# Kernel optimization log

Measured on AMD Instinct MI355X. Metric: run time of the kernel, lower is better.

## Reference

```python
import jax, jax.numpy as jnp
import numpy as np

NS, NV = 16, 4          # scalar / vector multiplicities (model defaults)
N_NODES, N_EDGES = 50000, 400000
WEIGHT_NUMEL = NS * NS + NS * NV  # 320: paths 0e*0e->0e and 0e*1o->1o


def sph_harm_l012(vec):
    """Real spherical harmonics l=0,1,2 with e3nn 'component' normalization,
    evaluated on the normalized edge vectors. Output [E, 9]."""
    eps = 1e-8
    r = vec / (jnp.linalg.norm(vec, axis=-1, keepdims=True) + eps)
    x, y, z = r[:, 0], r[:, 1], r[:, 2]
    sh0 = jnp.ones_like(x)[:, None]
    c1 = np.float32(np.sqrt(3.0))
    sh1 = c1 * jnp.stack([x, y, z], -1)
    c2 = np.float32(np.sqrt(15.0))
    c2b = np.float32(np.sqrt(5.0) / 2.0)
    sh2 = jnp.stack([c2 * x * y, c2 * y * z, c2b * (3 * z * z - 1.0),
                     c2 * z * x, 0.5 * c2 * (x * x - y * y)], -1)
    return jnp.concatenate([sh0, sh1, sh2], -1)


def setup_inputs() -> dict:
    key = jax.random.key(0)
    ks = jax.random.split(key, 8)
    h = 3 * NS  # n_edge_features = hidden_features = 48
    node_attr = jax.random.normal(ks[0], (N_NODES, NS), jnp.float32)
    edge_attr = jax.random.normal(ks[1], (N_EDGES, h), jnp.float32)
    edge_vec = jax.random.normal(ks[2], (N_EDGES, 3), jnp.float32)
    edge_index = jax.random.randint(ks[3], (2, N_EDGES), 0, N_NODES)
    fc1_w = jax.random.normal(ks[4], (h, h), jnp.float32) / np.sqrt(h)
    fc1_b = jnp.zeros((h,), jnp.float32)
    fc2_w = jax.random.normal(ks[5], (h, WEIGHT_NUMEL), jnp.float32) / np.sqrt(h)
    fc2_b = jnp.zeros((WEIGHT_NUMEL,), jnp.float32)
    return {"node_attr": node_attr, "edge_attr": edge_attr, "edge_vec": edge_vec,
            "fc1_w": fc1_w, "fc1_b": fc1_b, "fc2_w": fc2_w, "fc2_b": fc2_b,
            "edge_index": edge_index}


def reference(node_attr, edge_attr, edge_vec, fc1_w, fc1_b, fc2_w, fc2_b, edge_index):
    N = node_attr.shape[0]
    E = edge_attr.shape[0]
    edge_src, edge_dst = edge_index[0], edge_index[1]

    # spherical harmonics of edge directions (build_*_conv_graph)
    edge_sh = sph_harm_l012(edge_vec)                 # [E, 9]

    # per-edge TP weights: fc = Linear -> ReLU -> Linear (dropout=0)
    w = jax.nn.relu(edge_attr @ fc1_w + fc1_b) @ fc2_w + fc2_b  # [E, 320]
    w0 = w[:, :NS * NS].reshape(E, NS, NS)            # path 0e x 0e -> 0e
    w1 = w[:, NS * NS:].reshape(E, NS, NV)            # path 0e x 1o -> 1o

    # gather destination-node features
    x = node_attr[edge_dst]                           # [E, NS]

    # FullyConnectedTensorProduct('16x0e', sh, '16x0e + 4x1o'):
    # fan-in per output = NS (mul_u * mul_v summed over paths) -> 1/sqrt(NS)
    inv = np.float32(1.0 / np.sqrt(NS))
    out0 = jnp.einsum('euw,eu->ew', w0, x) * edge_sh[:, :1] * inv       # [E, NS]
    out1 = jnp.einsum('euw,eu,em->ewm', w1, x, edge_sh[:, 1:4]) * inv   # [E, NV, 3]
    msg = jnp.concatenate([out0, out1.reshape(E, NV * 3)], -1)          # [E, NS+3*NV]

    # scatter-mean over edge_src (reduce='mean', dim_size=N)
    summed = jax.ops.segment_sum(msg, edge_src, num_segments=N)
    cnt = jax.ops.segment_sum(jnp.ones((E,), msg.dtype), edge_src, num_segments=N)
    return summed / jnp.maximum(cnt, 1.0)[:, None]
```

## Files before the change

### kernel.cpp

```cpp
#include <hip/hip_runtime.h>
#include <hip/hip_bf16.h>
#include <math.h>

#define NS 16
#define H  48
#define TB 256
#define THREADS 512

typedef __attribute__((ext_vector_type(8))) short bf16x8;
typedef __attribute__((ext_vector_type(4))) float f32x4;

#define W2O   2304
#define B1H   20224
#define ZO    20272
#define ATO   20280
#define XO_   36664
#define SMEM_HW 40760
#define MSGF  10140
#define WCPY  2535

__device__ __forceinline__ short f2bf(float f) {
    unsigned b = __float_as_uint(f);
    unsigned r = (b + 0x7FFFu + ((b >> 16) & 1u)) >> 16;
    return (short)r;
}
__device__ __forceinline__ float bf2f(short s) {
    return __uint_as_float(((unsigned)(unsigned short)s) << 16);
}
__device__ __forceinline__ unsigned cvtpk(float lo, float hi) {
    unsigned r;
    asm("v_cvt_pk_bf16_f32 %0, %1, %2" : "=v"(r) : "v"(lo), "v"(hi));
    return r;
}
__device__ __forceinline__ uint4 pk8(float4 a, float4 b) {
    uint4 q;
    q.x = cvtpk(a.x, a.y); q.y = cvtpk(a.z, a.w);
    q.z = cvtpk(b.x, b.y); q.w = cvtpk(b.z, b.w);
    return q;
}

__global__ __launch_bounds__(256) void prep_hist_kernel(
    const float* __restrict__ fc1_w, const float* __restrict__ fc2_w,
    const float* __restrict__ fc1_b, const float* __restrict__ fc2_b,
    short* __restrict__ wpack,
    const int* __restrict__ edge_index, int* __restrict__ deg, int E)
{
    if (blockIdx.x < 6) {
        int t = blockIdx.x * 256 + threadIdx.x;
        if (t < 1472) {
            int f = t >> 6, l = t & 63;
            bool isW1 = (f < 3);
            int u = isW1 ? f : (f - 3);
            int n = u * 16 + (l & 15);
            const float* W = isW1 ? fc1_w : fc2_w;
            int ldw = isW1 ? 48 : 320;
            int base = isW1 ? (f * 768) : (W2O + u * 896);
            short* d0 = wpack + base + l * 8;
            #pragma unroll
            for (int i = 0; i < 8; ++i)
                d0[i] = f2bf(W[((l >> 4) * 8 + i) * ldw + n]);
            if (l < 32) {
                short* d1 = wpack + base + 512 + l * 8;
                #pragma unroll
                for (int i = 0; i < 8; ++i)
                    d1[i] = f2bf(W[(32 + (l >> 4) * 8 + i) * ldw + n]);
            } else if (!isW1 && l < 48) {
                short* d1 = wpack + base + 512 + l * 8;
                d1[0] = f2bf(fc2_b[n]);
                #pragma unroll
                for (int i = 1; i < 8; ++i) d1[i] = 0;
            }
        } else if (t < 1520) {
            wpack[B1H + (t - 1472)] = f2bf(fc1_b[t - 1472]);
        } else if (t < 1528) {
            wpack[ZO + (t - 1520)] = 0;
        }
    } else {
        int i = (blockIdx.x - 6) * 256 + threadIdx.x;
        if (i < E) atomicAdd(deg + edge_index[i], 1);
    }
}

__global__ __launch_bounds__(THREADS, 2) void edge_mfma_kernel(
    const float* __restrict__ node_attr,
    const float* __restrict__ edge_attr,
    const float* __restrict__ edge_vec,
    const short* __restrict__ wpack,
    const int*   __restrict__ edge_index,
    float* __restrict__ msg,
    int*   __restrict__ cursor,
    int E)
{
    __shared__ __align__(16) short smemS[SMEM_HW];
    float* smemF = (float*)smemS;
    const int tid = threadIdx.x;
    const int base = blockIdx.x * TB;
    const int l  = tid & 63;
    const int wv = tid >> 6;
    const int g  = l >> 4;
    const int c  = l & 15;
    const int rb = wv * 32;

    const int r = tid >> 1, h = tid & 1;
    const int e = base + r;
    const int ce = e < E ? e : (E - 1);
    const int sI_raw = edge_index[ce];
    const int dI = edge_index[E + ce];

    float shx_r = 0.f, shy_r = 0.f, shz_r = 0.f;
    int slot_r = 0;

    for (int idx = tid; idx < WCPY; idx += THREADS) {
        uint4 v = ((const uint4*)wpack)[idx];
        *(uint4*)&smemS[idx * 8] = v;
    }

    {
        const float* ap = edge_attr + (size_t)ce * H + h * 24;
        float4 A0 = *(const float4*)(ap + 0);
        float4 A1 = *(const float4*)(ap + 4);
        float4 A2 = *(const float4*)(ap + 8);
        float4 A3 = *(const float4*)(ap + 12);
        float4 A4 = *(const float4*)(ap + 16);
        float4 A5 = *(const float4*)(ap + 20);
        const float* xp = node_attr + (size_t)dI * NS + h * 8;
        float4 X0 = *(const float4*)(xp + 0);
        float4 X1 = *(const float4*)(xp + 4);
        if (e >= E) {
            A0 = make_float4(0,0,0,0); A1 = A0; A2 = A0; A3 = A0; A4 = A0; A5 = A0;
            X0 = A0; X1 = A0;
        }
        const int s8 = (r & 7) << 3;
        *(uint4*)&smemS[ATO + r * 64 + (((h*3 + 0) << 3) ^ s8)] = pk8(A0, A1);
        *(uint4*)&smemS[ATO + r * 64 + (((h*3 + 1) << 3) ^ s8)] = pk8(A2, A3);
        *(uint4*)&smemS[ATO + r * 64 + (((h*3 + 2) << 3) ^ s8)] = pk8(A4, A5);
        {
            int az = ATO + r * 64 + (((6 + h) << 3) ^ s8);
            uint4 zq;
            zq.x = (h == 0) ? 0x00003F80u : 0u;
            zq.y = 0u; zq.z = 0u; zq.w = 0u;
            *(uint4*)&smemS[az] = zq;
        }
        *(uint4*)&smemS[XO_ + r * 16 + h * 8] = pk8(X0, X1);
        if (h == 0) {
            int sI = (e < E) ? sI_raw : 0;
            float vx = 0.f, vy = 0.f, vz = 0.f;
            if (e < E) {
                vx = edge_vec[3 * (size_t)ce + 0];
                vy = edge_vec[3 * (size_t)ce + 1];
                vz = edge_vec[3 * (size_t)ce + 2];
            }
            float rn = 1.0f / (sqrtf(vx*vx + vy*vy + vz*vz) + 1e-8f);
            const float c1 = 1.7320508075688772f;
            shx_r = c1 * vx * rn; shy_r = c1 * vy * rn; shz_r = c1 * vz * rn;
            if (e < E) slot_r = atomicAdd(cursor + sI, 1);
        }
    }
    __syncthreads();

    bf16x8 a0[2], a1[2];
    #pragma unroll
    for (int m = 0; m < 2; ++m) {
        int row = rb + m * 16 + c, s8 = (row & 7) << 3;
        a0[m] = *(const bf16x8*)&smemS[ATO + row * 64 + ((g * 8) ^ s8)];
        a1[m] = *(const bf16x8*)&smemS[ATO + row * 64 + ((32 + g * 8) ^ s8)];
    }
    #pragma unroll
    for (int fr = 0; fr < 3; ++fr) {
        bf16x8 b0 = *(const bf16x8*)&smemS[fr * 768 + l * 8];
        bf16x8 b1 = *(const bf16x8*)&smemS[(l < 32) ? (fr * 768 + 512 + l * 8) : ZO];
        float bia = bf2f(smemS[B1H + fr * 16 + c]);
        #pragma unroll
        for (int m = 0; m < 2; ++m) {
            f32x4 acc = {0.f, 0.f, 0.f, 0.f};
            acc = __builtin_amdgcn_mfma_f32_16x16x32_bf16(a0[m], b0, acc, 0, 0, 0);
            acc = __builtin_amdgcn_mfma_f32_16x16x32_bf16(a1[m], b1, acc, 0, 0, 0);
            float t0 = fmaxf(acc[0] + bia, 0.f);
            float t1 = fmaxf(acc[1] + bia, 0.f);
            float t2 = fmaxf(acc[2] + bia, 0.f);
            float t3 = fmaxf(acc[3] + bia, 0.f);
            unsigned p01 = cvtpk(t0, t1);
            unsigned p23 = cvtpk(t2, t3);
            int row0 = rb + m * 16 + g * 4;
            int col = fr * 16 + c;
            smemS[ATO + (row0+0) * 64 + (col ^ (((row0+0) & 7) << 3))] = (short)p01;
            smemS[ATO + (row0+1) * 64 + (col ^ (((row0+1) & 7) << 3))] = (short)(p01 >> 16);
            smemS[ATO + (row0+2) * 64 + (col ^ (((row0+2) & 7) << 3))] = (short)p23;
            smemS[ATO + (row0+3) * 64 + (col ^ (((row0+3) & 7) << 3))] = (short)(p23 >> 16);
        }
    }

    bf16x8 tf0[2], tf1[2];
    #pragma unroll
    for (int m = 0; m < 2; ++m) {
        int row = rb + m * 16 + c, s8 = (row & 7) << 3;
        tf0[m] = *(const bf16x8*)&smemS[ATO + row * 64 + ((g * 8) ^ s8)];
        tf1[m] = *(const bf16x8*)&smemS[ATO + row * 64 + ((32 + g * 8) ^ s8)];
    }
    bf16x8 xr0[2][4], xr1[2][4];
    #pragma unroll
    for (int m = 0; m < 2; ++m)
        #pragma unroll
        for (int j = 0; j < 4; ++j) {
            int row = rb + m * 16 + g * 4 + j;
            xr0[m][j] = *(const bf16x8*)&smemS[XO_ + row * 16];
            xr1[m][j] = *(const bf16x8*)&smemS[XO_ + row * 16 + 8];
        }

    float o0[2][4] = {{0.f,0.f,0.f,0.f},{0.f,0.f,0.f,0.f}};
    float o1[2][4] = {{0.f,0.f,0.f,0.f},{0.f,0.f,0.f,0.f}};
    const int s2 = c >> 2;
    #pragma unroll
    for (int u = 0; u < 20; ++u) {
        const int wb = W2O + u * 896;
        bf16x8 b0 = *(const bf16x8*)&smemS[wb + l * 8];
        bf16x8 b1 = *(const bf16x8*)&smemS[(l < 48) ? (wb + 512 + l * 8) : ZO];
        #pragma unroll
        for (int m = 0; m < 2; ++m) {
            f32x4 acc = {0.f, 0.f, 0.f, 0.f};
            acc = __builtin_amdgcn_mfma_f32_16x16x32_bf16(tf0[m], b0, acc, 0, 0, 0);
            acc = __builtin_amdgcn_mfma_f32_16x16x32_bf16(tf1[m], b1, acc, 0, 0, 0);
            if (u < 16) {
                #pragma unroll
                for (int j = 0; j < 4; ++j) {
                    float xu = bf2f(u < 8 ? xr0[m][j][u] : xr1[m][j][u - 8]);
                    o0[m][j] = fmaf(xu, acc[j], o0[m][j]);
                }
            } else {
                const int f = u - 16;
                #pragma unroll
                for (int j = 0; j < 4; ++j) {
                    float e0, e1, e2, e3;
                    if (f < 2) {
                        e0 = bf2f(xr0[m][j][f*4+0]); e1 = bf2f(xr0[m][j][f*4+1]);
                        e2 = bf2f(xr0[m][j][f*4+2]); e3 = bf2f(xr0[m][j][f*4+3]);
                    } else {
                        e0 = bf2f(xr1[m][j][(f-2)*4+0]); e1 = bf2f(xr1[m][j][(f-2)*4+1]);
                        e2 = bf2f(xr1[m][j][(f-2)*4+2]); e3 = bf2f(xr1[m][j][(f-2)*4+3]);
                    }
                    float xu = e0;
                    xu = (s2 == 1) ? e1 : xu;
                    xu = (s2 == 2) ? e2 : xu;
                    xu = (s2 == 3) ? e3 : xu;
                    o1[m][j] = fmaf(xu, acc[j], o1[m][j]);
                }
            }
        }
    }
    #pragma unroll
    for (int m = 0; m < 2; ++m)
        #pragma unroll
        for (int j = 0; j < 4; ++j) {
            o1[m][j] += __shfl_xor(o1[m][j], 4);
            o1[m][j] += __shfl_xor(o1[m][j], 8);
        }

    const float inv = 0.25f;
    #pragma unroll
    for (int m = 0; m < 2; ++m)
        #pragma unroll
        for (int j = 0; j < 4; ++j) {
            const int rloc = m*16 + g*4 + j;
            const int rr = rb + rloc;
            const int srcl = rloc * 2;
            float shx = __shfl(shx_r, srcl);
            float shy = __shfl(shy_r, srcl);
            float shz = __shfl(shz_r, srcl);
            int lsrc = (g << 4) + (c < 12 ? c / 3 : 0);
            float ov = __shfl(o1[m][j], lsrc);
            int m3 = c - 3 * (c / 3);
            float shm = (m3 == 0) ? shx : ((m3 == 1) ? shy : shz);
            float v2 = (c < 12) ? ov * shm * inv : 0.f;
            smemF[MSGF + rr * 32 + c]      = o0[m][j] * inv;
            smemF[MSGF + rr * 32 + 16 + c] = v2;
        }

    #pragma unroll
    for (int it = 0; it < 4; ++it) {
        int rloc2 = it * 8 + (l >> 3);
        int r2 = rb + rloc2;
        int ch = (l & 7) * 4;
        int e2 = base + r2;
        int slot = __shfl(slot_r, rloc2 * 2);
        float4 val = *(const float4*)&smemF[MSGF + r2 * 32 + ch];
        if (e2 < E) *(float4*)(msg + (size_t)slot * 32 + ch) = val;
    }
}

__global__ __launch_bounds__(1024) void offsets_kernel(
    const int* __restrict__ deg, int* __restrict__ starts,
    int* __restrict__ cursor, int* __restrict__ gtotal, int N)
{
    __shared__ int lds[1024];
    __shared__ int base_s;
    const int t = threadIdx.x;
    const int i = blockIdx.x * 1024 + t;
    int v = (i < N) ? deg[i] : 0;
    lds[t] = v;
    __syncthreads();
    int acc = v;
    for (int off = 1; off < 1024; off <<= 1) {
        int u = (t >= off) ? lds[t - off] : 0;
        __syncthreads();
        acc += u;
        lds[t] = acc;
        __syncthreads();
    }
    if (t == 1023) base_s = atomicAdd(gtotal, acc);
    __syncthreads();
    int excl = acc - v;
    if (i < N) {
        int s = base_s + excl;
        starts[i] = s;
        cursor[i] = s;
    }
}

__global__ __launch_bounds__(256) void sum_kernel(
    const float* __restrict__ msg, const int* __restrict__ starts,
    const int* __restrict__ deg, float* __restrict__ out, int N)
{
    int n = (blockIdx.x * blockDim.x + threadIdx.x) >> 5;
    int ch = threadIdx.x & 31;
    if (n >= N) return;
    int s = starts[n], d = deg[n];
    const float* mb = msg + (size_t)s * 32 + ch;
    float a0 = 0.f, a1 = 0.f, a2 = 0.f, a3 = 0.f;
    int k = 0;
    for (; k + 4 <= d; k += 4) {
        a0 += mb[(size_t)(k + 0) * 32];
        a1 += mb[(size_t)(k + 1) * 32];
        a2 += mb[(size_t)(k + 2) * 32];
        a3 += mb[(size_t)(k + 3) * 32];
    }
    if (k + 2 <= d) {
        a0 += mb[(size_t)(k + 0) * 32];
        a1 += mb[(size_t)(k + 1) * 32];
        k += 2;
    }
    if (k < d) a2 += mb[(size_t)k * 32];
    float acc = (a0 + a1) + (a2 + a3);
    if (ch < 28) out[(size_t)n * 28 + ch] = acc / fmaxf((float)d, 1.0f);
}

__global__ __launch_bounds__(256) void finalize_kernel(
    float* __restrict__ out, const float* __restrict__ cnt, int total)
{
    int i = blockIdx.x * blockDim.x + threadIdx.x;
    if (i < total) {
        float cv = cnt[i / 28];
        out[i] = out[i] / fmaxf(cv, 1.0f);
    }
}

__global__ __launch_bounds__(256) void naive_kernel(
    const float* __restrict__ node_attr, const float* __restrict__ edge_attr,
    const float* __restrict__ edge_vec, const float* __restrict__ fc1_w,
    const float* __restrict__ fc1_b, const float* __restrict__ fc2_w,
    const float* __restrict__ fc2_b, const int* __restrict__ edge_index,
    float* __restrict__ out, float* __restrict__ cnt, int E)
{
    int e = blockIdx.x * blockDim.x + threadIdx.x;
    if (e >= E) return;
    float a[H];
    for (int i = 0; i < H; ++i) a[i] = edge_attr[(size_t)e*H + i];
    int dst = edge_index[E + e];
    float x[NS];
    for (int i = 0; i < NS; ++i) x[i] = node_attr[(size_t)dst*NS + i];
    float o0[NS] = {0}, o1v[4] = {0};
    for (int k = 0; k < H; ++k) {
        float tk = fc1_b[k];
        for (int j = 0; j < H; ++j) tk = fmaf(a[j], fc1_w[j*H + k], tk);
        tk = fmaxf(tk, 0.f);
        const float* row = fc2_w + k*320;
        for (int u = 0; u < NS; ++u) {
            float q = tk * x[u];
            for (int w = 0; w < NS; ++w) o0[w] = fmaf(q, row[u*NS+w], o0[w]);
            for (int v = 0; v < 4; ++v) o1v[v] = fmaf(q, row[256+u*4+v], o1v[v]);
        }
    }
    for (int u = 0; u < NS; ++u) {
        float xu = x[u];
        for (int w = 0; w < NS; ++w) o0[w] = fmaf(xu, fc2_b[u*NS+w], o0[w]);
        for (int v = 0; v < 4; ++v) o1v[v] = fmaf(xu, fc2_b[256+u*4+v], o1v[v]);
    }
    float vx = edge_vec[3*(size_t)e], vy = edge_vec[3*(size_t)e+1], vz = edge_vec[3*(size_t)e+2];
    float rn = 1.0f / (sqrtf(vx*vx+vy*vy+vz*vz) + 1e-8f);
    const float c1 = 1.7320508075688772f;
    float sx = c1*vx*rn, sy = c1*vy*rn, sz = c1*vz*rn;
    int src = edge_index[e];
    float* ob = out + (size_t)src * 28;
    for (int w = 0; w < NS; ++w) atomicAdd(ob + w, o0[w] * 0.25f);
    for (int v = 0; v < 4; ++v) {
        float q = o1v[v] * 0.25f;
        atomicAdd(ob + 16 + 3*v + 0, q * sx);
        atomicAdd(ob + 16 + 3*v + 1, q * sy);
        atomicAdd(ob + 16 + 3*v + 2, q * sz);
    }
    atomicAdd(cnt + src, 1.0f);
}

extern "C" void kernel_launch(void* const* d_in, const int* in_sizes, int n_in,
                              void* d_out, int out_size, void* d_ws, size_t ws_size,
                              hipStream_t stream) {
    const float* node_attr  = (const float*)d_in[0];
    const float* edge_attr  = (const float*)d_in[1];
    const float* edge_vec   = (const float*)d_in[2];
    const float* fc1_w      = (const float*)d_in[3];
    const float* fc1_b      = (const float*)d_in[4];
    const float* fc2_w      = (const float*)d_in[5];
    const float* fc2_b      = (const float*)d_in[6];
    const int*   edge_index = (const int*)d_in[7];

    int E = in_sizes[2] / 3;
    int N = in_sizes[0] / NS;
    float* out = (float*)d_out;

    size_t msg_b  = (size_t)E * 32 * sizeof(float);
    size_t ints_b = (3 * (size_t)N + 1) * sizeof(int);
    size_t wpk_b  = (size_t)WCPY * 16;
    size_t need   = msg_b + ints_b + wpk_b;

    if (ws_size >= need) {
        float* msg  = (float*)d_ws;
        int* ip     = (int*)((char*)d_ws + msg_b);
        int* deg    = ip;
        int* gtotal = ip + N;
        int* starts = ip + N + 1;
        int* cursor = ip + 2 * N + 1;
        short* wpack = (short*)((char*)d_ws + msg_b + ints_b);

        hipMemsetAsync(deg, 0, ((size_t)N + 1) * sizeof(int), stream);
        int nhist = (E + 255) / 256;
        prep_hist_kernel<<<6 + nhist, 256, 0, stream>>>(
            fc1_w, fc2_w, fc1_b, fc2_b, wpack, edge_index, deg, E);
        offsets_kernel<<<(N + 1023) / 1024, 1024, 0, stream>>>(
            deg, starts, cursor, gtotal, N);
        edge_mfma_kernel<<<(E + TB - 1) / TB, THREADS, 0, stream>>>(
            node_attr, edge_attr, edge_vec, wpack, edge_index, msg, cursor, E);
        sum_kernel<<<((size_t)N * 32 + 255) / 256, 256, 0, stream>>>(
            msg, starts, deg, out, N);
    } else {
        float* cnt = (float*)d_ws;
        hipMemsetAsync(d_out, 0, (size_t)out_size * sizeof(float), stream);
        hipMemsetAsync(d_ws, 0, (size_t)N * sizeof(float), stream);
        naive_kernel<<<(E + 255) / 256, 256, 0, stream>>>(
            node_attr, edge_attr, edge_vec, fc1_w, fc1_b, fc2_w, fc2_b,
            edge_index, out, cnt, E);
        int total = N * 28;
        finalize_kernel<<<(total + 255) / 256, 256, 0, stream>>>(out, cnt, total);
    }
}
```

Measured before the change: 104.4 us.

## Shrink edge tile to 64 edges per block with four loader threads per edge

Shrinks each block from 256 edges on 512 threads to 64 edges on 256 threads, so every wave handles one 16-row MFMA tile instead of two. Loading changes to four threads per edge: three threads fetch edge_attr slices and the fourth fetches node features, the edge vector and the zero padding. The goal is lower register and LDS use per block, which allows more resident blocks and more latency hiding on the gathers. The trade-off is that the 2535-vector packed weight table is copied into LDS by four times as many blocks, each with half the threads, and each B fragment loaded from LDS now feeds one MFMA tile instead of two.

```diff
diff --git a/kernel.cpp b/kernel.cpp
--- a/kernel.cpp
+++ b/kernel.cpp
@@ -4,8 +4,8 @@
 
 #define NS 16
 #define H  48
-#define TB 256
-#define THREADS 512
+#define TB 64
+#define THREADS 256
 
 typedef __attribute__((ext_vector_type(8))) short bf16x8;
 typedef __attribute__((ext_vector_type(4))) float f32x4;
@@ -14,8 +14,8 @@
 #define B1H   20224
 #define ZO    20272
 #define ATO   20280
-#define XO_   36664
-#define SMEM_HW 40760
+#define XO_   24376
+#define SMEM_HW 25400
 #define MSGF  10140
 #define WCPY  2535
 
@@ -99,9 +99,9 @@
     const int wv = tid >> 6;
     const int g  = l >> 4;
     const int c  = l & 15;
-    const int rb = wv * 32;
-
-    const int r = tid >> 1, h = tid & 1;
+    const int rb = wv * 16;
+
+    const int r = tid >> 2, h = tid & 3;
     const int e = base + r;
     const int ce = e < E ? e : (E - 1);
     const int sI_raw = edge_index[ce];
@@ -116,34 +116,31 @@
     }
 
     {
-        const float* ap = edge_attr + (size_t)ce * H + h * 24;
-        float4 A0 = *(const float4*)(ap + 0);
-        float4 A1 = *(const float4*)(ap + 4);
-        float4 A2 = *(const float4*)(ap + 8);
-        float4 A3 = *(const float4*)(ap + 12);
-        float4 A4 = *(const float4*)(ap + 16);
-        float4 A5 = *(const float4*)(ap + 20);
-        const float* xp = node_attr + (size_t)dI * NS + h * 8;
-        float4 X0 = *(const float4*)(xp + 0);
-        float4 X1 = *(const float4*)(xp + 4);
-        if (e >= E) {
-            A0 = make_float4(0,0,0,0); A1 = A0; A2 = A0; A3 = A0; A4 = A0; A5 = A0;
-            X0 = A0; X1 = A0;
-        }
         const int s8 = (r & 7) << 3;
-        *(uint4*)&smemS[ATO + r * 64 + (((h*3 + 0) << 3) ^ s8)] = pk8(A0, A1);
-        *(uint4*)&smemS[ATO + r * 64 + (((h*3 + 1) << 3) ^ s8)] = pk8(A2, A3);
-        *(uint4*)&smemS[ATO + r * 64 + (((h*3 + 2) << 3) ^ s8)] = pk8(A4, A5);
-        {
-            int az = ATO + r * 64 + (((6 + h) << 3) ^ s8);
-            uint4 zq;
-            zq.x = (h == 0) ? 0x00003F80u : 0u;
-            zq.y = 0u; zq.z = 0u; zq.w = 0u;
-            *(uint4*)&smemS[az] = zq;
-        }
-        *(uint4*)&smemS[XO_ + r * 16 + h * 8] = pk8(X0, X1);
-        if (h == 0) {
-            int sI = (e < E) ? sI_raw : 0;
+        if (h < 3) {
+            const float* ap = edge_attr + (size_t)ce * H + h * 16;
+            float4 A0 = *(const float4*)(ap + 0);
+            float4 A1 = *(const float4*)(ap + 4);
+            float4 A2 = *(const float4*)(ap + 8);
+            float4 A3 = *(const float4*)(ap + 12);
+            if (e >= E) {
+                A0 = make_float4(0,0,0,0); A1 = A0; A2 = A0; A3 = A0;
+            }
+            *(uint4*)&smemS[ATO + r * 64 + (((2*h + 0) << 3) ^ s8)] = pk8(A0, A1);
+            *(uint4*)&smemS[ATO + r * 64 + (((2*h + 1) << 3) ^ s8)] = pk8(A2, A3);
+        } else {
+            uint4 zq; zq.x = 0x00003F80u; zq.y = 0u; zq.z = 0u; zq.w = 0u;
+            uint4 zz; zz.x = 0u; zz.y = 0u; zz.z = 0u; zz.w = 0u;
+            *(uint4*)&smemS[ATO + r * 64 + ((6 << 3) ^ s8)] = zq;
+            *(uint4*)&smemS[ATO + r * 64 + ((7 << 3) ^ s8)] = zz;
+            const float* xp = node_attr + (size_t)dI * NS;
+            float4 X0 = *(const float4*)(xp + 0);
+            float4 X1 = *(const float4*)(xp + 4);
+            float4 X2 = *(const float4*)(xp + 8);
+            float4 X3 = *(const float4*)(xp + 12);
+            if (e >= E) { X0 = make_float4(0,0,0,0); X1 = X0; X2 = X0; X3 = X0; }
+            *(uint4*)&smemS[XO_ + r * 16 + 0] = pk8(X0, X1);
+            *(uint4*)&smemS[XO_ + r * 16 + 8] = pk8(X2, X3);
             float vx = 0.f, vy = 0.f, vz = 0.f;
             if (e < E) {
                 vx = edge_vec[3 * (size_t)ce + 0];
@@ -153,135 +150,113 @@
             float rn = 1.0f / (sqrtf(vx*vx + vy*vy + vz*vz) + 1e-8f);
             const float c1 = 1.7320508075688772f;
             shx_r = c1 * vx * rn; shy_r = c1 * vy * rn; shz_r = c1 * vz * rn;
-            if (e < E) slot_r = atomicAdd(cursor + sI, 1);
         }
+        if (h == 0 && e < E) slot_r = atomicAdd(cursor + sI_raw, 1);
     }
     __syncthreads();
 
-    bf16x8 a0[2], a1[2];
-    #pragma unroll
-    for (int m = 0; m < 2; ++m) {
-        int row = rb + m * 16 + c, s8 = (row & 7) << 3;
-        a0[m] = *(const bf16x8*)&smemS[ATO + row * 64 + ((g * 8) ^ s8)];
-        a1[m] = *(const bf16x8*)&smemS[ATO + row * 64 + ((32 + g * 8) ^ s8)];
-    }
+    const int rowA = rb + c, s8a = (rowA & 7) << 3;
+    bf16x8 a0 = *(const bf16x8*)&smemS[ATO + rowA * 64 + ((g * 8) ^ s8a)];
+    bf16x8 a1 = *(const bf16x8*)&smemS[ATO + rowA * 64 + ((32 + g * 8) ^ s8a)];
     #pragma unroll
     for (int fr = 0; fr < 3; ++fr) {
         bf16x8 b0 = *(const bf16x8*)&smemS[fr * 768 + l * 8];
         bf16x8 b1 = *(const bf16x8*)&smemS[(l < 32) ? (fr * 768 + 512 + l * 8) : ZO];
         float bia = bf2f(smemS[B1H + fr * 16 + c]);
-        #pragma unroll
-        for (int m = 0; m < 2; ++m) {
-            f32x4 acc = {0.f, 0.f, 0.f, 0.f};
-            acc = __builtin_amdgcn_mfma_f32_16x16x32_bf16(a0[m], b0, acc, 0, 0, 0);
-            acc = __builtin_amdgcn_mfma_f32_16x16x32_bf16(a1[m], b1, acc, 0, 0, 0);
-            float t0 = fmaxf(acc[0] + bia, 0.f);
-            float t1 = fmaxf(acc[1] + bia, 0.f);
-            float t2 = fmaxf(acc[2] + bia, 0.f);
-            float t3 = fmaxf(acc[3] + bia, 0.f);
-            unsigned p01 = cvtpk(t0, t1);
-            unsigned p23 = cvtpk(t2, t3);
-            int row0 = rb + m * 16 + g * 4;
-            int col = fr * 16 + c;
-            smemS[ATO + (row0+0) * 64 + (col ^ (((row0+0) & 7) << 3))] = (short)p01;
-            smemS[ATO + (row0+1) * 64 + (col ^ (((row0+1) & 7) << 3))] = (short)(p01 >> 16);
-            smemS[ATO + (row0+2) * 64 + (col ^ (((row0+2) & 7) << 3))] = (short)p23;
-            smemS[ATO + (row0+3) * 64 + (col ^ (((row0+3) & 7) << 3))] = (short)(p23 >> 16);
-        }
-    }
-
-    bf16x8 tf0[2], tf1[2];
-    #pragma unroll
-    for (int m = 0; m < 2; ++m) {
-        int row = rb + m * 16 + c, s8 = (row & 7) << 3;
-        tf0[m] = *(const bf16x8*)&smemS[ATO + row * 64 + ((g * 8) ^ s8)];
-        tf1[m] = *(const bf16x8*)&smemS[ATO + row * 64 + ((32 + g * 8) ^ s8)];
-    }
-    bf16x8 xr0[2][4], xr1[2][4];
-    #pragma unroll
-    for (int m = 0; m < 2; ++m)
-        #pragma unroll
-        for (int j = 0; j < 4; ++j) {
-            int row = rb + m * 16 + g * 4 + j;
-            xr0[m][j] = *(const bf16x8*)&smemS[XO_ + row * 16];
-            xr1[m][j] = *(const bf16x8*)&smemS[XO_ + row * 16 + 8];
-        }
-
-    float o0[2][4] = {{0.f,0.f,0.f,0.f},{0.f,0.f,0.f,0.f}};
-    float o1[2][4] = {{0.f,0.f,0.f,0.f},{0.f,0.f,0.f,0.f}};
+        f32x4 acc = {0.f, 0.f, 0.f, 0.f};
+        acc = __builtin_amdgcn_mfma_f32_16x16x32_bf16(a0, b0, acc, 0, 0, 0);
+        acc = __builtin_amdgcn_mfma_f32_16x16x32_bf16(a1, b1, acc, 0, 0, 0);
+        float t0 = fmaxf(acc[0] + bia, 0.f);
+        float t1 = fmaxf(acc[1] + bia, 0.f);
+        float t2 = fmaxf(acc[2] + bia, 0.f);
+        float t3 = fmaxf(acc[3] + bia, 0.f);
+        unsigned p01 = cvtpk(t0, t1);
+        unsigned p23 = cvtpk(t2, t3);
+        int row0 = rb + g * 4;
+        int col = fr * 16 + c;
+        smemS[ATO + (row0+0) * 64 + (col ^ (((row0+0) & 7) << 3))] = (short)p01;
+        smemS[ATO + (row0+1) * 64 + (col ^ (((row0+1) & 7) << 3))] = (short)(p01 >> 16);
+        smemS[ATO + (row0+2) * 64 + (col ^ (((row0+2) & 7) << 3))] = (short)p23;
+        smemS[ATO + (row0+3) * 64 + (col ^ (((row0+3) & 7) << 3))] = (short)(p23 >> 16);
+    }
+
+    bf16x8 tf0 = *(const bf16x8*)&smemS[ATO + rowA * 64 + ((g * 8) ^ s8a)];
+    bf16x8 tf1 = *(const bf16x8*)&smemS[ATO + rowA * 64 + ((32 + g * 8) ^ s8a)];
+    bf16x8 xr0[4], xr1[4];
+    #pragma unroll
+    for (int j = 0; j < 4; ++j) {
+        int row = rb + g * 4 + j;
+        xr0[j] = *(const bf16x8*)&smemS[XO_ + row * 16];
+        xr1[j] = *(const bf16x8*)&smemS[XO_ + row * 16 + 8];
+    }
+
+    float o0[4] = {0.f, 0.f, 0.f, 0.f};
+    float o1[4] = {0.f, 0.f, 0.f, 0.f};
     const int s2 = c >> 2;
     #pragma unroll
     for (int u = 0; u < 20; ++u) {
         const int wb = W2O + u * 896;
         bf16x8 b0 = *(const bf16x8*)&smemS[wb + l * 8];
         bf16x8 b1 = *(const bf16x8*)&smemS[(l < 48) ? (wb + 512 + l * 8) : ZO];
-        #pragma unroll
-        for (int m = 0; m < 2; ++m) {
-            f32x4 acc = {0.f, 0.f, 0.f, 0.f};
-            acc = __builtin_amdgcn_mfma_f32_16x16x32_bf16(tf0[m], b0, acc, 0, 0, 0);
-            acc = __builtin_amdgcn_mfma_f32_16x16x32_bf16(tf1[m], b1, acc, 0, 0, 0);
-            if (u < 16) {
-                #pragma unroll
-                for (int j = 0; j < 4; ++j) {
-                    float xu = bf2f(u < 8 ? xr0[m][j][u] : xr1[m][j][u - 8]);
-                    o0[m][j] = fmaf(xu, acc[j], o0[m][j]);
+        f32x4 acc = {0.f, 0.f, 0.f, 0.f};
+        acc = __builtin_amdgcn_mfma_f32_16x16x32_bf16(tf0, b0, acc, 0, 0, 0);
+        acc = __builtin_amdgcn_mfma_f32_16x16x32_bf16(tf1, b1, acc, 0, 0, 0);
+        if (u < 16) {
+            #pragma unroll
+            for (int j = 0; j < 4; ++j) {
+                float xu = bf2f(u < 8 ? xr0[j][u] : xr1[j][u - 8]);
+                o0[j] = fmaf(xu, acc[j], o0[j]);
+            }
+        } else {
+            const int f = u - 16;
+            #pragma unroll
+            for (int j = 0; j < 4; ++j) {
+                float e0, e1, e2, e3;
+                if (f < 2) {
+                    e0 = bf2f(xr0[j][f*4+0]); e1 = bf2f(xr0[j][f*4+1]);
+                    e2 = bf2f(xr0[j][f*4+2]); e3 = bf2f(xr0[j][f*4+3]);
+                } else {
+                    e0 = bf2f(xr1[j][(f-2)*4+0]); e1 = bf2f(xr1[j][(f-2)*4+1]);
+                    e2 = bf2f(xr1[j][(f-2)*4+2]); e3 = bf2f(xr1[j][(f-2)*4+3]);
                 }
-            } else {
-                const int f = u - 16;
-                #pragma unroll
-                for (int j = 0; j < 4; ++j) {
-                    float e0, e1, e2, e3;
-                    if (f < 2) {
-                        e0 = bf2f(xr0[m][j][f*4+0]); e1 = bf2f(xr0[m][j][f*4+1]);
-                        e2 = bf2f(xr0[m][j][f*4+2]); e3 = bf2f(xr0[m][j][f*4+3]);
-                    } else {
-                        e0 = bf2f(xr1[m][j][(f-2)*4+0]); e1 = bf2f(xr1[m][j][(f-2)*4+1]);
-                        e2 = bf2f(xr1[m][j][(f-2)*4+2]); e3 = bf2f(xr1[m][j][(f-2)*4+3]);
-                    }
-                    float xu = e0;
-                    xu = (s2 == 1) ? e1 : xu;
-                    xu = (s2 == 2) ? e2 : xu;
-                    xu = (s2 == 3) ? e3 : xu;
-                    o1[m][j] = fmaf(xu, acc[j], o1[m][j]);
-                }
+                float xu = e0;
+                xu = (s2 == 1) ? e1 : xu;
+                xu = (s2 == 2) ? e2 : xu;
+                xu = (s2 == 3) ? e3 : xu;
+                o1[j] = fmaf(xu, acc[j], o1[j]);
             }
         }
     }
     #pragma unroll
-    for (int m = 0; m < 2; ++m)
-        #pragma unroll
-        for (int j = 0; j < 4; ++j) {
-            o1[m][j] += __shfl_xor(o1[m][j], 4);
-            o1[m][j] += __shfl_xor(o1[m][j], 8);
-        }
+    for (int j = 0; j < 4; ++j) {
+        o1[j] += __shfl_xor(o1[j], 4);
+        o1[j] += __shfl_xor(o1[j], 8);
+    }
 
     const float inv = 0.25f;
     #pragma unroll
-    for (int m = 0; m < 2; ++m)
-        #pragma unroll
-        for (int j = 0; j < 4; ++j) {
-            const int rloc = m*16 + g*4 + j;
-            const int rr = rb + rloc;
-            const int srcl = rloc * 2;
-            float shx = __shfl(shx_r, srcl);
-            float shy = __shfl(shy_r, srcl);
-            float shz = __shfl(shz_r, srcl);
-            int lsrc = (g << 4) + (c < 12 ? c / 3 : 0);
-            float ov = __shfl(o1[m][j], lsrc);
-            int m3 = c - 3 * (c / 3);
-            float shm = (m3 == 0) ? shx : ((m3 == 1) ? shy : shz);
-            float v2 = (c < 12) ? ov * shm * inv : 0.f;
-            smemF[MSGF + rr * 32 + c]      = o0[m][j] * inv;
-            smemF[MSGF + rr * 32 + 16 + c] = v2;
-        }
-
-    #pragma unroll
-    for (int it = 0; it < 4; ++it) {
+    for (int j = 0; j < 4; ++j) {
+        const int rloc = g * 4 + j;
+        const int rr = rb + rloc;
+        float shx = __shfl(shx_r, rloc * 4 + 3);
+        float shy = __shfl(shy_r, rloc * 4 + 3);
+        float shz = __shfl(shz_r, rloc * 4 + 3);
+        int lsrc = (g << 4) + (c < 12 ? c / 3 : 0);
+        float ov = __shfl(o1[j], lsrc);
+        int m3 = c - 3 * (c / 3);
+        float shm = (m3 == 0) ? shx : ((m3 == 1) ? shy : shz);
+        float v2 = (c < 12) ? ov * shm * inv : 0.f;
+        smemF[MSGF + rr * 32 + c]      = o0[j] * inv;
+        smemF[MSGF + rr * 32 + 16 + c] = v2;
+    }
+
+    #pragma unroll
+    for (int it = 0; it < 2; ++it) {
         int rloc2 = it * 8 + (l >> 3);
         int r2 = rb + rloc2;
         int ch = (l & 7) * 4;
         int e2 = base + r2;
-        int slot = __shfl(slot_r, rloc2 * 2);
+        int slot = __shfl(slot_r, rloc2 * 4);
         float4 val = *(const float4*)&smemF[MSGF + r2 * 32 + ch];
         if (e2 < E) *(float4*)(msg + (size_t)slot * 32 + ch) = val;
     }
```

Result: slower. 109.5 us (+4.9%).

## Process 512 edges per block with one edge per thread

Applied to the files above, without the earlier changes.

Doubles the edges handled per block from 256 to 512, so each thread loads a full edge row and each wave runs four MFMA row tiles instead of two. The goal is to amortize the per-block copy of the packed weights into shared memory over more edges and to reuse each B fragment across more MFMAs. In exchange, shared memory per block grows, launch bounds drop to one block per SM, and register pressure rises with the larger accumulator and operand arrays, which cuts occupancy and latency hiding for the gather loads.

```diff
diff --git a/kernel.cpp b/kernel.cpp
--- a/kernel.cpp
+++ b/kernel.cpp
@@ -4,7 +4,7 @@
 
 #define NS 16
 #define H  48
-#define TB 256
+#define TB 512
 #define THREADS 512
 
 typedef __attribute__((ext_vector_type(8))) short bf16x8;
@@ -14,8 +14,8 @@
 #define B1H   20224
 #define ZO    20272
 #define ATO   20280
-#define XO_   36664
-#define SMEM_HW 40760
+#define XO_   53048
+#define SMEM_HW 61240
 #define MSGF  10140
 #define WCPY  2535
 
@@ -81,7 +81,7 @@
     }
 }
 
-__global__ __launch_bounds__(THREADS, 2) void edge_mfma_kernel(
+__global__ __launch_bounds__(THREADS, 1) void edge_mfma_kernel(
     const float* __restrict__ node_attr,
     const float* __restrict__ edge_attr,
     const float* __restrict__ edge_vec,
@@ -99,9 +99,9 @@
     const int wv = tid >> 6;
     const int g  = l >> 4;
     const int c  = l & 15;
-    const int rb = wv * 32;
-
-    const int r = tid >> 1, h = tid & 1;
+    const int rb = wv * 64;
+
+    const int r = tid;
     const int e = base + r;
     const int ce = e < E ? e : (E - 1);
     const int sI_raw = edge_index[ce];
@@ -116,51 +116,60 @@
     }
 
     {
-        const float* ap = edge_attr + (size_t)ce * H + h * 24;
+        const float* ap = edge_attr + (size_t)ce * H;
         float4 A0 = *(const float4*)(ap + 0);
         float4 A1 = *(const float4*)(ap + 4);
         float4 A2 = *(const float4*)(ap + 8);
         float4 A3 = *(const float4*)(ap + 12);
         float4 A4 = *(const float4*)(ap + 16);
         float4 A5 = *(const float4*)(ap + 20);
-        const float* xp = node_attr + (size_t)dI * NS + h * 8;
+        float4 A6 = *(const float4*)(ap + 24);
+        float4 A7 = *(const float4*)(ap + 28);
+        float4 A8 = *(const float4*)(ap + 32);
+        float4 A9 = *(const float4*)(ap + 36);
+        float4 Aa = *(const float4*)(ap + 40);
+        float4 Ab = *(const float4*)(ap + 44);
+        const float* xp = node_attr + (size_t)dI * NS;
         float4 X0 = *(const float4*)(xp + 0);
         float4 X1 = *(const float4*)(xp + 4);
+        float4 X2 = *(const float4*)(xp + 8);
+        float4 X3 = *(const float4*)(xp + 12);
         if (e >= E) {
             A0 = make_float4(0,0,0,0); A1 = A0; A2 = A0; A3 = A0; A4 = A0; A5 = A0;
-            X0 = A0; X1 = A0;
+            A6 = A0; A7 = A0; A8 = A0; A9 = A0; Aa = A0; Ab = A0;
+            X0 = A0; X1 = A0; X2 = A0; X3 = A0;
         }
         const int s8 = (r & 7) << 3;
-        *(uint4*)&smemS[ATO + r * 64 + (((h*3 + 0) << 3) ^ s8)] = pk8(A0, A1);
-        *(uint4*)&smemS[ATO + r * 64 + (((h*3 + 1) << 3) ^ s8)] = pk8(A2, A3);
-        *(uint4*)&smemS[ATO + r * 64 + (((h*3 + 2) << 3) ^ s8)] = pk8(A4, A5);
+        *(uint4*)&smemS[ATO + r * 64 + ((0 << 3) ^ s8)] = pk8(A0, A1);
+        *(uint4*)&smemS[ATO + r * 64 + ((1 << 3) ^ s8)] = pk8(A2, A3);
+        *(uint4*)&smemS[ATO + r * 64 + ((2 << 3) ^ s8)] = pk8(A4, A5);
+        *(uint4*)&smemS[ATO + r * 64 + ((3 << 3) ^ s8)] = pk8(A6, A7);
+        *(uint4*)&smemS[ATO + r * 64 + ((4 << 3) ^ s8)] = pk8(A8, A9);
+        *(uint4*)&smemS[ATO + r * 64 + ((5 << 3) ^ s8)] = pk8(Aa, Ab);
         {
-            int az = ATO + r * 64 + (((6 + h) << 3) ^ s8);
-            uint4 zq;
-            zq.x = (h == 0) ? 0x00003F80u : 0u;
-            zq.y = 0u; zq.z = 0u; zq.w = 0u;
-            *(uint4*)&smemS[az] = zq;
-        }
-        *(uint4*)&smemS[XO_ + r * 16 + h * 8] = pk8(X0, X1);
-        if (h == 0) {
-            int sI = (e < E) ? sI_raw : 0;
-            float vx = 0.f, vy = 0.f, vz = 0.f;
-            if (e < E) {
-                vx = edge_vec[3 * (size_t)ce + 0];
-                vy = edge_vec[3 * (size_t)ce + 1];
-                vz = edge_vec[3 * (size_t)ce + 2];
-            }
-            float rn = 1.0f / (sqrtf(vx*vx + vy*vy + vz*vz) + 1e-8f);
-            const float c1 = 1.7320508075688772f;
-            shx_r = c1 * vx * rn; shy_r = c1 * vy * rn; shz_r = c1 * vz * rn;
-            if (e < E) slot_r = atomicAdd(cursor + sI, 1);
-        }
+            uint4 zq; zq.x = 0x00003F80u; zq.y = 0u; zq.z = 0u; zq.w = 0u;
+            uint4 zz; zz.x = 0u; zz.y = 0u; zz.z = 0u; zz.w = 0u;
+            *(uint4*)&smemS[ATO + r * 64 + ((6 << 3) ^ s8)] = zq;
+            *(uint4*)&smemS[ATO + r * 64 + ((7 << 3) ^ s8)] = zz;
+        }
+        *(uint4*)&smemS[XO_ + r * 16 + 0] = pk8(X0, X1);
+        *(uint4*)&smemS[XO_ + r * 16 + 8] = pk8(X2, X3);
+        float vx = 0.f, vy = 0.f, vz = 0.f;
+        if (e < E) {
+            vx = edge_vec[3 * (size_t)ce + 0];
+            vy = edge_vec[3 * (size_t)ce + 1];
+            vz = edge_vec[3 * (size_t)ce + 2];
+        }
+        float rn = 1.0f / (sqrtf(vx*vx + vy*vy + vz*vz) + 1e-8f);
+        const float c1 = 1.7320508075688772f;
+        shx_r = c1 * vx * rn; shy_r = c1 * vy * rn; shz_r = c1 * vz * rn;
+        if (e < E) slot_r = atomicAdd(cursor + sI_raw, 1);
     }
     __syncthreads();
 
-    bf16x8 a0[2], a1[2];
-    #pragma unroll
-    for (int m = 0; m < 2; ++m) {
+    bf16x8 a0[4], a1[4];
+    #pragma unroll
+    for (int m = 0; m < 4; ++m) {
         int row = rb + m * 16 + c, s8 = (row & 7) << 3;
         a0[m] = *(const bf16x8*)&smemS[ATO + row * 64 + ((g * 8) ^ s8)];
         a1[m] = *(const bf16x8*)&smemS[ATO + row * 64 + ((32 + g * 8) ^ s8)];
@@ -171,7 +180,7 @@
         bf16x8 b1 = *(const bf16x8*)&smemS[(l < 32) ? (fr * 768 + 512 + l * 8) : ZO];
         float bia = bf2f(smemS[B1H + fr * 16 + c]);
         #pragma unroll
-        for (int m = 0; m < 2; ++m) {
+        for (int m = 0; m < 4; ++m) {
             f32x4 acc = {0.f, 0.f, 0.f, 0.f};
             acc = __builtin_amdgcn_mfma_f32_16x16x32_bf16(a0[m], b0, acc, 0, 0, 0);
             acc = __builtin_amdgcn_mfma_f32_16x16x32_bf16(a1[m], b1, acc, 0, 0, 0);
@@ -190,16 +199,16 @@
         }
     }
 
-    bf16x8 tf0[2], tf1[2];
-    #pragma unroll
-    for (int m = 0; m < 2; ++m) {
+    bf16x8 tf0[4], tf1[4];
+    #pragma unroll
+    for (int m = 0; m < 4; ++m) {
         int row = rb + m * 16 + c, s8 = (row & 7) << 3;
         tf0[m] = *(const bf16x8*)&smemS[ATO + row * 64 + ((g * 8) ^ s8)];
         tf1[m] = *(const bf16x8*)&smemS[ATO + row * 64 + ((32 + g * 8) ^ s8)];
     }
-    bf16x8 xr0[2][4], xr1[2][4];
-    #pragma unroll
-    for (int m = 0; m < 2; ++m)
+    bf16x8 xr0[4][4], xr1[4][4];
+    #pragma unroll
+    for (int m = 0; m < 4; ++m)
         #pragma unroll
         for (int j = 0; j < 4; ++j) {
             int row = rb + m * 16 + g * 4 + j;
@@ -207,8 +216,8 @@
             xr1[m][j] = *(const bf16x8*)&smemS[XO_ + row * 16 + 8];
         }
 
-    float o0[2][4] = {{0.f,0.f,0.f,0.f},{0.f,0.f,0.f,0.f}};
-    float o1[2][4] = {{0.f,0.f,0.f,0.f},{0.f,0.f,0.f,0.f}};
+    float o0[4][4] = {{0,0,0,0},{0,0,0,0},{0,0,0,0},{0,0,0,0}};
+    float o1[4][4] = {{0,0,0,0},{0,0,0,0},{0,0,0,0},{0,0,0,0}};
     const int s2 = c >> 2;
     #pragma unroll
     for (int u = 0; u < 20; ++u) {
@@ -216,7 +225,7 @@
         bf16x8 b0 = *(const bf16x8*)&smemS[wb + l * 8];
         bf16x8 b1 = *(const bf16x8*)&smemS[(l < 48) ? (wb + 512 + l * 8) : ZO];
         #pragma unroll
-        for (int m = 0; m < 2; ++m) {
+        for (int m = 0; m < 4; ++m) {
             f32x4 acc = {0.f, 0.f, 0.f, 0.f};
             acc = __builtin_amdgcn_mfma_f32_16x16x32_bf16(tf0[m], b0, acc, 0, 0, 0);
             acc = __builtin_amdgcn_mfma_f32_16x16x32_bf16(tf1[m], b1, acc, 0, 0, 0);
@@ -248,7 +257,7 @@
         }
     }
     #pragma unroll
-    for (int m = 0; m < 2; ++m)
+    for (int m = 0; m < 4; ++m)
         #pragma unroll
         for (int j = 0; j < 4; ++j) {
             o1[m][j] += __shfl_xor(o1[m][j], 4);
@@ -257,15 +266,14 @@
 
     const float inv = 0.25f;
     #pragma unroll
-    for (int m = 0; m < 2; ++m)
+    for (int m = 0; m < 4; ++m)
         #pragma unroll
         for (int j = 0; j < 4; ++j) {
             const int rloc = m*16 + g*4 + j;
             const int rr = rb + rloc;
-            const int srcl = rloc * 2;
-            float shx = __shfl(shx_r, srcl);
-            float shy = __shfl(shy_r, srcl);
-            float shz = __shfl(shz_r, srcl);
+            float shx = __shfl(shx_r, rloc);
+            float shy = __shfl(shy_r, rloc);
+            float shz = __shfl(shz_r, rloc);
             int lsrc = (g << 4) + (c < 12 ? c / 3 : 0);
             float ov = __shfl(o1[m][j], lsrc);
             int m3 = c - 3 * (c / 3);
@@ -276,12 +284,12 @@
         }
 
     #pragma unroll
-    for (int it = 0; it < 4; ++it) {
+    for (int it = 0; it < 8; ++it) {
         int rloc2 = it * 8 + (l >> 3);
         int r2 = rb + rloc2;
         int ch = (l & 7) * 4;
         int e2 = base + r2;
-        int slot = __shfl(slot_r, rloc2 * 2);
+        int slot = __shfl(slot_r, rloc2);
         float4 val = *(const float4*)&smemF[MSGF + r2 * 32 + ch];
         if (e2 < E) *(float4*)(msg + (size_t)slot * 32 + ch) = val;
     }
```

After: 124.1 us. 18.9% more time.
